# Kernel tuning notes

Hardware: AMD Instinct MI355X
Metric: run time of the kernel (lower is better)

Reference implementation:

```python
import jax, jax.numpy as jnp
import numpy as np

D_MODEL = 1024
NUM_HEADS = 16
D_K = D_MODEL // NUM_HEADS


def setup_inputs() -> dict:
    key = jax.random.key(0)
    ks = jax.random.split(key, 11)
    B, S = 4, 2048
    s = 1.0 / np.sqrt(D_MODEL)
    inp = {
        "q": jax.random.normal(ks[0], (B, S, D_MODEL), jnp.float32),
        "k": jax.random.normal(ks[1], (B, S, D_MODEL), jnp.float32),
        "v": jax.random.normal(ks[2], (B, S, D_MODEL), jnp.float32),
        "Wq": jax.random.normal(ks[3], (D_MODEL, D_MODEL), jnp.float32) * s,
        "bq": jnp.zeros((D_MODEL,), jnp.float32),
        "Wk": jax.random.normal(ks[4], (D_MODEL, D_MODEL), jnp.float32) * s,
        "bk": jnp.zeros((D_MODEL,), jnp.float32),
        "Wv": jax.random.normal(ks[5], (D_MODEL, D_MODEL), jnp.float32) * s,
        "bv": jnp.zeros((D_MODEL,), jnp.float32),
        "Wo": jax.random.normal(ks[6], (D_MODEL, D_MODEL), jnp.float32) * s,
        "bo": jnp.zeros((D_MODEL,), jnp.float32),
    }
    return inp


def reference(q, k, v, Wq, bq, Wk, bk, Wv, bv, Wo, bo):
    B, S, _ = q.shape
    # QKV projections, then split heads: [B,S,D] -> [B,H,S,d_k]
    def split_heads(x):
        return x.reshape(B, -1, NUM_HEADS, D_K).transpose(0, 2, 1, 3)
    Q = split_heads(q @ Wq + bq)
    K = split_heads(k @ Wk + bk)
    V = split_heads(v @ Wv + bv)
    # scaled dot-product attention (mask=None, dropout p=0 -> identity)
    scores = jnp.einsum("bhqd,bhkd->bhqk", Q, K) / jnp.sqrt(jnp.float32(D_K))
    attn = jax.nn.softmax(scores, axis=-1)
    out = jnp.einsum("bhqk,bhkd->bhqd", attn, V)
    out = out.transpose(0, 2, 1, 3).reshape(B, -1, D_MODEL)
    return out @ Wo + bo
```

## Files before the change

kernel.cpp:

```cpp
#include <hip/hip_runtime.h>

#define MB (1ull << 20)

typedef __attribute__((ext_vector_type(8))) short bf16x8;
typedef __attribute__((ext_vector_type(4))) float f32x4;

#if defined(__has_builtin)
#if __has_builtin(__builtin_amdgcn_global_load_lds)
#define HAS_GLL 1
#endif
#endif
#ifndef HAS_GLL
#define HAS_GLL 0
#endif

__device__ __forceinline__ unsigned short f2bf(float f) {
  unsigned u = __float_as_uint(f);
  u += 0x7fffu + ((u >> 16) & 1u);
  return (unsigned short)(u >> 16);
}

#if HAS_GLL
__device__ __forceinline__ void gl16(const unsigned short* g, unsigned short* l) {
  __builtin_amdgcn_global_load_lds((const __attribute__((address_space(1))) void*)g,
                                   (__attribute__((address_space(3))) void*)l, 16, 0, 0);
}
#endif

__global__ __launch_bounds__(256) void cvt3(const float* __restrict__ x0,
                                            const float* __restrict__ x1,
                                            const float* __restrict__ x2,
                                            unsigned short* __restrict__ y0,
                                            unsigned short* __restrict__ y1,
                                            unsigned short* __restrict__ y2, int n) {
  const int z = blockIdx.y;
  const float* x = (z == 0) ? x0 : (z == 1) ? x1 : x2;
  unsigned short* y = (z == 0) ? y0 : (z == 1) ? y1 : y2;
  int i = (blockIdx.x * 256 + threadIdx.x) * 4;
  if (i >= n) return;
  float4 v = *(const float4*)(x + i);
  uint2 p;
  p.x = (unsigned)f2bf(v.x) | ((unsigned)f2bf(v.y) << 16);
  p.y = (unsigned)f2bf(v.z) | ((unsigned)f2bf(v.w) << 16);
  *(uint2*)(y + i) = p;
}

__global__ __launch_bounds__(256) void transpose4(const float* __restrict__ W0,
                                                  const float* __restrict__ W1,
                                                  const float* __restrict__ W2,
                                                  const float* __restrict__ W3,
                                                  unsigned short* __restrict__ T0,
                                                  unsigned short* __restrict__ T1,
                                                  unsigned short* __restrict__ T2,
                                                  unsigned short* __restrict__ T3) {
  const int z = blockIdx.z;
  const float* W = (z == 0) ? W0 : (z == 1) ? W1 : (z == 2) ? W2 : W3;
  unsigned short* WT = (z == 0) ? T0 : (z == 1) ? T1 : (z == 2) ? T2 : T3;
  __shared__ float tile[32][33];
  int bx = blockIdx.x * 32;
  int by = blockIdx.y * 32;
  int tx = threadIdx.x & 31, ty = threadIdx.x >> 5;
#pragma unroll
  for (int i = 0; i < 32; i += 8)
    tile[ty + i][tx] = W[(by + ty + i) * 1024 + bx + tx];
  __syncthreads();
#pragma unroll
  for (int i = 0; i < 32; i += 8)
    WT[(bx + ty + i) * 1024 + by + tx] = f2bf(tile[tx][ty + i]);
}

__device__ __forceinline__ void gemm_core(const unsigned short* __restrict__ A,
                                          const unsigned short* __restrict__ Bt, int K, int m0,
                                          int n0, unsigned short* As, unsigned short* Bs,
                                          f32x4 (&acc)[4][4]) {
  const int tid = threadIdx.x;
  const int wave = tid >> 6, lane = tid & 63;
  const int quad = lane >> 4, r = lane & 15;
  const int wm = (wave >> 1) * 64, wn = (wave & 1) * 64;

  const int srow8 = tid >> 3;
  const int clog8 = ((tid & 7) ^ (srow8 & 7)) * 8;
  const unsigned short* Ag = A + (size_t)(m0 + srow8) * K + clog8;
  const unsigned short* Bg = Bt + (size_t)(n0 + srow8) * K + clog8;

  const int cA = ((0 ^ quad) ^ (r & 7)) * 8;
  const int cB = ((4 ^ quad) ^ (r & 7)) * 8;

  for (int k0 = 0; k0 < K; k0 += 64) {
    __syncthreads();
#if HAS_GLL
#pragma unroll
    for (int s = 0; s < 4; ++s) {
      gl16(Ag + (size_t)(s * 32) * K + k0, As + s * 2048 + tid * 8);
      gl16(Bg + (size_t)(s * 32) * K + k0, Bs + s * 2048 + tid * 8);
    }
#else
#pragma unroll
    for (int s = 0; s < 4; ++s) {
      uint4 a = *(const uint4*)(Ag + (size_t)(s * 32) * K + k0);
      uint4 b = *(const uint4*)(Bg + (size_t)(s * 32) * K + k0);
      *(uint4*)(As + s * 2048 + tid * 8) = a;
      *(uint4*)(Bs + s * 2048 + tid * 8) = b;
    }
#endif
    __syncthreads();
#pragma unroll
    for (int ks = 0; ks < 2; ++ks) {
      const int co = ks ? cB : cA;
      bf16x8 af[4], bfr[4];
#pragma unroll
      for (int i = 0; i < 4; ++i) af[i] = *(const bf16x8*)(As + (wm + i * 16 + r) * 64 + co);
#pragma unroll
      for (int j = 0; j < 4; ++j) bfr[j] = *(const bf16x8*)(Bs + (wn + j * 16 + r) * 64 + co);
#pragma unroll
      for (int i = 0; i < 4; ++i)
#pragma unroll
        for (int j = 0; j < 4; ++j)
          acc[i][j] = __builtin_amdgcn_mfma_f32_16x16x32_bf16(af[i], bfr[j], acc[i][j], 0, 0, 0);
    }
  }
}

__global__ __launch_bounds__(256) void gemm_qkv(
    const unsigned short* __restrict__ A0, const unsigned short* __restrict__ A1,
    const unsigned short* __restrict__ A2, const unsigned short* __restrict__ B0,
    const unsigned short* __restrict__ B1, const unsigned short* __restrict__ B2,
    const float* __restrict__ b0, const float* __restrict__ b1, const float* __restrict__ b2,
    unsigned short* __restrict__ O0, unsigned short* __restrict__ O1,
    unsigned short* __restrict__ O2, int M, int N, int K, float scaleQ) {
  __shared__ __align__(16) unsigned short As[128 * 64];
  __shared__ __align__(16) unsigned short Bs[128 * 64];
  const int z = blockIdx.z;
  const unsigned short* A = (z == 0) ? A0 : (z == 1) ? A1 : A2;
  const unsigned short* Bt = (z == 0) ? B0 : (z == 1) ? B1 : B2;
  const float* bias = (z == 0) ? b0 : (z == 1) ? b1 : b2;
  const float scale = (z == 0) ? scaleQ : 1.0f;
  const int m0 = blockIdx.y * 128, n0 = blockIdx.x * 128;

  f32x4 acc[4][4] = {};
  gemm_core(A, Bt, K, m0, n0, As, Bs, acc);

  const int lane = threadIdx.x & 63, wave = threadIdx.x >> 6;
  const int quad = lane >> 4, r = lane & 15;
  const int wm = (wave >> 1) * 64, wn = (wave & 1) * 64;

  if (z < 2) {
    unsigned short* Cout = (z == 0) ? O0 : O1;
#pragma unroll
    for (int i = 0; i < 4; ++i)
#pragma unroll
      for (int j = 0; j < 4; ++j) {
        const int col = n0 + wn + j * 16 + r;
        const float bv = bias[col];
#pragma unroll
        for (int t = 0; t < 4; ++t) {
          const int row = m0 + wm + i * 16 + quad * 4 + t;
          Cout[(size_t)row * N + col] = f2bf((acc[i][j][t] + bv) * scale);
        }
      }
  } else {
    const int b = m0 >> 11;
#pragma unroll
    for (int i = 0; i < 4; ++i)
#pragma unroll
      for (int j = 0; j < 4; ++j) {
        const int col = n0 + wn + j * 16 + r;
        const float bv = bias[col];
        const int rloc = (m0 & 2047) + wm + i * 16 + quad * 4;
        uint2 u;
        u.x = ((unsigned)f2bf(acc[i][j][1] + bv) << 16) | f2bf(acc[i][j][0] + bv);
        u.y = ((unsigned)f2bf(acc[i][j][3] + bv) << 16) | f2bf(acc[i][j][2] + bv);
        *(uint2*)(O2 + ((size_t)(b * N + col)) * 2048 + rloc) = u;
      }
  }
}

__global__ __launch_bounds__(256) void gemm_o(const unsigned short* __restrict__ A,
                                              const unsigned short* __restrict__ Bt,
                                              const float* __restrict__ bias,
                                              float* __restrict__ Cout, int M, int N, int K) {
  __shared__ __align__(16) unsigned short As[128 * 64];
  __shared__ __align__(16) unsigned short Bs[128 * 64];
  const int m0 = blockIdx.y * 128, n0 = blockIdx.x * 128;
  f32x4 acc[4][4] = {};
  gemm_core(A, Bt, K, m0, n0, As, Bs, acc);

  const int lane = threadIdx.x & 63, wave = threadIdx.x >> 6;
  const int quad = lane >> 4, r = lane & 15;
  const int wm = (wave >> 1) * 64, wn = (wave & 1) * 64;
#pragma unroll
  for (int i = 0; i < 4; ++i)
#pragma unroll
    for (int j = 0; j < 4; ++j) {
      const int col = n0 + wn + j * 16 + r;
      const float bv = bias[col];
#pragma unroll
      for (int t = 0; t < 4; ++t) {
        const int row = m0 + wm + i * 16 + quad * 4 + t;
        Cout[(size_t)row * N + col] = acc[i][j][t] + bv;
      }
    }
}

__global__ __launch_bounds__(256) void flash_mfma(const unsigned short* __restrict__ Qb,
                                                  const unsigned short* __restrict__ Kb,
                                                  const unsigned short* __restrict__ Vt,
                                                  unsigned short* __restrict__ Ob) {
  __shared__ __align__(16) unsigned short Ksh[64 * 72];
  __shared__ __align__(16) unsigned short Vts[64 * 72];
  __shared__ __align__(16) unsigned short Ps[4 * 64 * 72];
  const int tid = threadIdx.x;
  const int wave = tid >> 6, lane = tid & 63;
  const int quad = lane >> 4, r = lane & 15;
  const int b = blockIdx.y >> 4, h = blockIdx.y & 15;
  const int qbase = b * 2048 + blockIdx.x * 256 + wave * 64;

  bf16x8 qf[4][2];
#pragma unroll
  for (int jq = 0; jq < 4; ++jq)
#pragma unroll
    for (int ks = 0; ks < 2; ++ks)
      qf[jq][ks] = *(const bf16x8*)(Qb + (size_t)(qbase + jq * 16 + r) * 1024 + h * 64 +
                                    ks * 32 + quad * 8);

  f32x4 oacc[4][4] = {};
  float lp[4] = {0.f, 0.f, 0.f, 0.f};

  const int srow = tid >> 2, sc = (tid & 3) * 16;
  const unsigned short* Kg = Kb + (size_t)(b * 2048 + srow) * 1024 + h * 64 + sc;
  const unsigned short* Vg = Vt + (size_t)(b * 1024 + h * 64 + srow) * 2048 + sc;
  unsigned short* PsW = Ps + wave * (64 * 72);

  for (int kt0 = 0; kt0 < 32; ++kt0) {
    uint4 ka = *(const uint4*)Kg;
    uint4 kb2 = *(const uint4*)(Kg + 8);
    uint4 va = *(const uint4*)Vg;
    uint4 vb2 = *(const uint4*)(Vg + 8);
    Kg += 64 * 1024;
    Vg += 64;
    __syncthreads();
    *(uint4*)(Ksh + srow * 72 + sc) = ka;
    *(uint4*)(Ksh + srow * 72 + sc + 8) = kb2;
    *(uint4*)(Vts + srow * 72 + sc) = va;
    *(uint4*)(Vts + srow * 72 + sc + 8) = vb2;
    __syncthreads();

    bf16x8 kf[4][2];
#pragma unroll
    for (int kt = 0; kt < 4; ++kt)
#pragma unroll
      for (int ks = 0; ks < 2; ++ks)
        kf[kt][ks] = *(const bf16x8*)(Ksh + (kt * 16 + r) * 72 + ks * 32 + quad * 8);

#pragma unroll
    for (int jq = 0; jq < 4; ++jq) {
      f32x4 st[4] = {};
#pragma unroll
      for (int ks = 0; ks < 2; ++ks)
#pragma unroll
        for (int kt = 0; kt < 4; ++kt)
          st[kt] = __builtin_amdgcn_mfma_f32_16x16x32_bf16(kf[kt][ks], qf[jq][ks], st[kt], 0, 0, 0);
#pragma unroll
      for (int kt = 0; kt < 4; ++kt) {
        float p0 = __builtin_amdgcn_exp2f(st[kt][0]);
        float p1 = __builtin_amdgcn_exp2f(st[kt][1]);
        float p2 = __builtin_amdgcn_exp2f(st[kt][2]);
        float p3 = __builtin_amdgcn_exp2f(st[kt][3]);
        lp[jq] += (p0 + p1) + (p2 + p3);
        uint2 u;
        u.x = __builtin_amdgcn_perm(__float_as_uint(p1) + 0x8000u,
                                    __float_as_uint(p0) + 0x8000u, 0x07060302u);
        u.y = __builtin_amdgcn_perm(__float_as_uint(p3) + 0x8000u,
                                    __float_as_uint(p2) + 0x8000u, 0x07060302u);
        *(uint2*)(PsW + (jq * 16 + r) * 72 + kt * 16 + quad * 4) = u;
      }
    }

    bf16x8 vf[4][2];
#pragma unroll
    for (int dt = 0; dt < 4; ++dt)
#pragma unroll
      for (int ks = 0; ks < 2; ++ks)
        vf[dt][ks] = *(const bf16x8*)(Vts + (dt * 16 + r) * 72 + ks * 32 + quad * 8);
#pragma unroll
    for (int jq = 0; jq < 4; ++jq)
#pragma unroll
      for (int ks = 0; ks < 2; ++ks) {
        bf16x8 pf = *(const bf16x8*)(PsW + (jq * 16 + r) * 72 + ks * 32 + quad * 8);
#pragma unroll
        for (int dt = 0; dt < 4; ++dt)
          oacc[jq][dt] =
              __builtin_amdgcn_mfma_f32_16x16x32_bf16(vf[dt][ks], pf, oacc[jq][dt], 0, 0, 0);
      }
  }

#pragma unroll
  for (int jq = 0; jq < 4; ++jq) {
    float l = lp[jq];
    l += __shfl_xor(l, 16);
    l += __shfl_xor(l, 32);
    float inv = 1.0f / l;
#pragma unroll
    for (int dt = 0; dt < 4; ++dt) {
      uint2 u;
      u.x = ((unsigned)f2bf(oacc[jq][dt][1] * inv) << 16) | f2bf(oacc[jq][dt][0] * inv);
      u.y = ((unsigned)f2bf(oacc[jq][dt][3] * inv) << 16) | f2bf(oacc[jq][dt][2] * inv);
      *(uint2*)(Ob + (size_t)(qbase + jq * 16 + r) * 1024 + h * 64 + dt * 16 + quad * 4) = u;
    }
  }
}

extern "C" void kernel_launch(void* const* d_in, const int* in_sizes, int n_in, void* d_out,
                              int out_size, void* d_ws, size_t ws_size, hipStream_t stream) {
  const float* q = (const float*)d_in[0];
  const float* k = (const float*)d_in[1];
  const float* v = (const float*)d_in[2];
  const float* Wq = (const float*)d_in[3];
  const float* bq = (const float*)d_in[4];
  const float* Wk = (const float*)d_in[5];
  const float* bk = (const float*)d_in[6];
  const float* Wv = (const float*)d_in[7];
  const float* bv = (const float*)d_in[8];
  const float* Wo = (const float*)d_in[9];
  const float* bo = (const float*)d_in[10];

  unsigned char* ws = (unsigned char*)d_ws;
  unsigned short* qb = (unsigned short*)(ws + 0 * MB);
  unsigned short* kb = (unsigned short*)(ws + 16 * MB);
  unsigned short* vb = (unsigned short*)(ws + 32 * MB);
  unsigned short* WqT = (unsigned short*)(ws + 48 * MB);
  unsigned short* WkT = (unsigned short*)(ws + 50 * MB);
  unsigned short* WvT = (unsigned short*)(ws + 52 * MB);
  unsigned short* WoT = (unsigned short*)(ws + 54 * MB);
  unsigned short* Qb = (unsigned short*)(ws + 56 * MB);
  unsigned short* Kbf = (unsigned short*)(ws + 72 * MB);
  unsigned short* Vtr = (unsigned short*)(ws + 88 * MB);
  unsigned short* AOb = (unsigned short*)(ws + 104 * MB);

  const int M = 8192, D = 1024;
  const float c2 = 0.18033688011112042f;

  cvt3<<<dim3(M * D / 1024, 3), 256, 0, stream>>>(q, k, v, qb, kb, vb, M * D);
  transpose4<<<dim3(32, 32, 4), 256, 0, stream>>>(Wq, Wk, Wv, Wo, WqT, WkT, WvT, WoT);

  gemm_qkv<<<dim3(D / 128, M / 128, 3), 256, 0, stream>>>(qb, kb, vb, WqT, WkT, WvT, bq, bk, bv,
                                                          Qb, Kbf, Vtr, M, D, D, c2);

  flash_mfma<<<dim3(8, 64), 256, 0, stream>>>(Qb, Kbf, Vtr, AOb);

  gemm_o<<<dim3(D / 128, M / 128), 256, 0, stream>>>(AOb, WoT, bo, (float*)d_out, M, D, D);
}
```

Before: 356.0 us.

## Keep softmax probabilities in registers using 16x16x16 MFMA for PV product

In the flash attention kernel, the P tile is no longer written to and re-read from LDS. The bf16-packed probabilities from the QK^T MFMA output layout feed the 16x16x16 bf16 MFMA directly as the A operand, with V fragments read in a matching layout, which transposes the output accumulator. The epilogue changes to match, using a shuffle for the row sums and scalar bf16 stores. The GEMM kernels also get a launch_bounds occupancy hint of 4 blocks. This trades the LDS round trip and the large Ps buffer for twice as many smaller MFMA instructions and less coalesced output stores.

After: 375.1 us. 1.05x slower.

```diff
diff --git a/kernel.cpp b/kernel.cpp
--- a/kernel.cpp
+++ b/kernel.cpp
@@ -3,15 +3,22 @@
 #define MB (1ull << 20)
 
 typedef __attribute__((ext_vector_type(8))) short bf16x8;
+typedef __attribute__((ext_vector_type(4))) short bf16x4;
 typedef __attribute__((ext_vector_type(4))) float f32x4;
 
 #if defined(__has_builtin)
 #if __has_builtin(__builtin_amdgcn_global_load_lds)
 #define HAS_GLL 1
 #endif
+#if __has_builtin(__builtin_amdgcn_mfma_f32_16x16x16bf16_1k)
+#define HAS_MFMA16 1
+#endif
 #endif
 #ifndef HAS_GLL
 #define HAS_GLL 0
+#endif
+#ifndef HAS_MFMA16
+#define HAS_MFMA16 0
 #endif
 
 __device__ __forceinline__ unsigned short f2bf(float f) {
@@ -121,7 +128,7 @@
   }
 }
 
-__global__ __launch_bounds__(256) void gemm_qkv(
+__global__ __launch_bounds__(256, 4) void gemm_qkv(
     const unsigned short* __restrict__ A0, const unsigned short* __restrict__ A1,
     const unsigned short* __restrict__ A2, const unsigned short* __restrict__ B0,
     const unsigned short* __restrict__ B1, const unsigned short* __restrict__ B2,
@@ -175,10 +182,10 @@
   }
 }
 
-__global__ __launch_bounds__(256) void gemm_o(const unsigned short* __restrict__ A,
-                                              const unsigned short* __restrict__ Bt,
-                                              const float* __restrict__ bias,
-                                              float* __restrict__ Cout, int M, int N, int K) {
+__global__ __launch_bounds__(256, 4) void gemm_o(const unsigned short* __restrict__ A,
+                                                 const unsigned short* __restrict__ Bt,
+                                                 const float* __restrict__ bias,
+                                                 float* __restrict__ Cout, int M, int N, int K) {
   __shared__ __align__(16) unsigned short As[128 * 64];
   __shared__ __align__(16) unsigned short Bs[128 * 64];
   const int m0 = blockIdx.y * 128, n0 = blockIdx.x * 128;
@@ -208,7 +215,9 @@
                                                   unsigned short* __restrict__ Ob) {
   __shared__ __align__(16) unsigned short Ksh[64 * 72];
   __shared__ __align__(16) unsigned short Vts[64 * 72];
+#if !HAS_MFMA16
   __shared__ __align__(16) unsigned short Ps[4 * 64 * 72];
+#endif
   const int tid = threadIdx.x;
   const int wave = tid >> 6, lane = tid & 63;
   const int quad = lane >> 4, r = lane & 15;
@@ -229,7 +238,9 @@
   const int srow = tid >> 2, sc = (tid & 3) * 16;
   const unsigned short* Kg = Kb + (size_t)(b * 2048 + srow) * 1024 + h * 64 + sc;
   const unsigned short* Vg = Vt + (size_t)(b * 1024 + h * 64 + srow) * 2048 + sc;
+#if !HAS_MFMA16
   unsigned short* PsW = Ps + wave * (64 * 72);
+#endif
 
   for (int kt0 = 0; kt0 < 32; ++kt0) {
     uint4 ka = *(const uint4*)Kg;
@@ -252,6 +263,9 @@
       for (int ks = 0; ks < 2; ++ks)
         kf[kt][ks] = *(const bf16x8*)(Ksh + (kt * 16 + r) * 72 + ks * 32 + quad * 8);
 
+#if HAS_MFMA16
+    bf16x4 pA[4][4];
+#endif
 #pragma unroll
     for (int jq = 0; jq < 4; ++jq) {
       f32x4 st[4] = {};
@@ -267,15 +281,36 @@
         float p2 = __builtin_amdgcn_exp2f(st[kt][2]);
         float p3 = __builtin_amdgcn_exp2f(st[kt][3]);
         lp[jq] += (p0 + p1) + (p2 + p3);
-        uint2 u;
-        u.x = __builtin_amdgcn_perm(__float_as_uint(p1) + 0x8000u,
-                                    __float_as_uint(p0) + 0x8000u, 0x07060302u);
-        u.y = __builtin_amdgcn_perm(__float_as_uint(p3) + 0x8000u,
-                                    __float_as_uint(p2) + 0x8000u, 0x07060302u);
-        *(uint2*)(PsW + (jq * 16 + r) * 72 + kt * 16 + quad * 4) = u;
-      }
-    }
-
+        unsigned lo = __builtin_amdgcn_perm(__float_as_uint(p1) + 0x8000u,
+                                            __float_as_uint(p0) + 0x8000u, 0x07060302u);
+        unsigned hi = __builtin_amdgcn_perm(__float_as_uint(p3) + 0x8000u,
+                                            __float_as_uint(p2) + 0x8000u, 0x07060302u);
+#if HAS_MFMA16
+        union { unsigned u[2]; bf16x4 v; } cv;
+        cv.u[0] = lo;
+        cv.u[1] = hi;
+        pA[jq][kt] = cv.v;
+#else
+        *(uint2*)(PsW + (jq * 16 + r) * 72 + kt * 16 + quad * 4) = make_uint2(lo, hi);
+#endif
+      }
+    }
+
+#if HAS_MFMA16
+#pragma unroll
+    for (int dt = 0; dt < 4; ++dt) {
+      bf16x4 vfB[4];
+#pragma unroll
+      for (int kt = 0; kt < 4; ++kt)
+        vfB[kt] = *(const bf16x4*)(Vts + (dt * 16 + r) * 72 + kt * 16 + quad * 4);
+#pragma unroll
+      for (int jq = 0; jq < 4; ++jq)
+#pragma unroll
+        for (int kt = 0; kt < 4; ++kt)
+          oacc[jq][dt] =
+              __builtin_amdgcn_mfma_f32_16x16x16bf16_1k(pA[jq][kt], vfB[kt], oacc[jq][dt], 0, 0, 0);
+    }
+#else
     bf16x8 vf[4][2];
 #pragma unroll
     for (int dt = 0; dt < 4; ++dt)
@@ -292,6 +327,7 @@
           oacc[jq][dt] =
               __builtin_amdgcn_mfma_f32_16x16x32_bf16(vf[dt][ks], pf, oacc[jq][dt], 0, 0, 0);
       }
+#endif
   }
 
 #pragma unroll
@@ -299,6 +335,18 @@
     float l = lp[jq];
     l += __shfl_xor(l, 16);
     l += __shfl_xor(l, 32);
+#if HAS_MFMA16
+#pragma unroll
+    for (int t = 0; t < 4; ++t) {
+      float lq = __shfl(l, quad * 4 + t);
+      float inv = 1.0f / lq;
+#pragma unroll
+      for (int dt = 0; dt < 4; ++dt) {
+        float v = oacc[jq][dt][t] * inv;
+        Ob[(size_t)(qbase + jq * 16 + quad * 4 + t) * 1024 + h * 64 + dt * 16 + r] = f2bf(v);
+      }
+    }
+#else
     float inv = 1.0f / l;
 #pragma unroll
     for (int dt = 0; dt < 4; ++dt) {
@@ -307,6 +355,7 @@
       u.y = ((unsigned)f2bf(oacc[jq][dt][3] * inv) << 16) | f2bf(oacc[jq][dt][2] * inv);
       *(uint2*)(Ob + (size_t)(qbase + jq * 16 + r) * 1024 + h * 64 + dt * 16 + quad * 4) = u;
     }
+#endif
   }
 }
 
```
